# Performance work log

Hardware: AMD Instinct MI355X
Metric: run time of the kernel (lower is better)

Reference implementation:

```python
import jax, jax.numpy as jnp
import numpy as np

COORD_W, EDGE_W, COUNT_W, REG_W, CONTRA_W = 1.0, 2.0, 0.1, 0.001, 0.1
MARGIN = 1.0


def setup_inputs() -> dict:
    key = jax.random.key(0)
    ks = jax.random.split(key, 6)
    B, N, D, C = 16, 1024, 128, 2
    return {
        "predicted_coords": jax.random.normal(ks[0], (B, N, C), jnp.float32),
        "points": jax.random.normal(ks[1], (B, N, C), jnp.float32),
        "adjacency_logits": jax.random.normal(ks[2], (B, N, N), jnp.float32),
        "adjacency": jax.random.bernoulli(ks[3], 0.1, (B, N, N)).astype(jnp.float32),
        "node_masks": jnp.ones((B, N), jnp.float32),  # all nodes valid -> n_actual = N
        "predicted_count": jax.random.normal(ks[4], (B, 1), jnp.float32),
        "node_features": jax.random.normal(ks[5], (B, N, D), jnp.float32),
    }


def _bce_with_logits(logits, targets):
    # mean-reduced, numerically stable (matches F.binary_cross_entropy_with_logits)
    return jnp.mean(jnp.maximum(logits, 0.0) - logits * targets
                    + jnp.log1p(jnp.exp(-jnp.abs(logits))))


def _smooth_l1(pred, target):
    d = jnp.abs(pred - target)
    return jnp.mean(jnp.where(d < 1.0, 0.5 * d * d, d - 0.5))


def _contrastive_sample(features, adj):
    # features: [N, D], adj: [N, N]. torch.cdist pairwise euclidean via gram trick.
    nrm = jnp.sum(features * features, axis=-1)              # [N]
    sq = jnp.maximum(nrm[:, None] + nrm[None, :]
                     - 2.0 * (features @ features.T), 0.0)   # [N, N] squared dists
    n = features.shape[0]
    eye = jnp.eye(n, dtype=bool)
    pos_mask = adj > 0.5
    neg_mask = (adj <= 0.5) & (~eye)
    # positive term: mean of distances**2 over positive pairs == mean squared dist
    pos = jnp.sum(jnp.where(pos_mask, sq, 0.0)) / jnp.maximum(jnp.sum(pos_mask), 1)
    dist = jnp.sqrt(jnp.maximum(sq, 1e-12))
    hinge = jnp.square(jax.nn.relu(MARGIN - dist))
    neg = jnp.sum(jnp.where(neg_mask, hinge, 0.0)) / jnp.maximum(jnp.sum(neg_mask), 1)
    return pos + neg


def reference(predicted_coords, points, adjacency_logits, adjacency,
              node_masks, predicted_count, node_features):
    # node_masks are all ones, so the per-sample [:n_actual] slicing is the
    # full tensor; per-sample MSE/BCE means averaged over batch equal global means.
    coord_loss = jnp.mean(jnp.square(predicted_coords - points))
    edge_loss = _bce_with_logits(adjacency_logits, adjacency)
    actual_counts = jnp.sum(node_masks, axis=1)              # [B]
    count_loss = _smooth_l1(predicted_count[:, 0], actual_counts)
    reg_loss = jnp.mean(jnp.square(node_features))
    # contrastive path uses targets['adjacency'] (no predicted_adjacency key)
    contra_loss = jnp.mean(jax.vmap(_contrastive_sample)(node_features, adjacency))
    total = (COORD_W * coord_loss + EDGE_W * edge_loss + COUNT_W * count_loss
             + REG_W * reg_loss + CONTRA_W * contra_loss)
    return total, coord_loss, edge_loss, count_loss, reg_loss, contra_loss
```

## Files before the change

### kernel.cpp

```cpp
#include <hip/hip_runtime.h>
#include <hip/hip_bf16.h>

#define NN 1024
#define DD 128
#define TS 64
#define PITCH 136

#define WS_COORD 0
#define WS_REG   1
#define WS_BCE   2
#define WS_POSN  3
#define WS_POSC  19
#define WS_NEGS  35
#define WS_PDIAG 51
#define WS_CROSS 67
#define WS_CNT   83
#define WS_NORM  112

typedef __bf16 bf16_t;
typedef bf16_t bf16x8 __attribute__((ext_vector_type(8)));
typedef float  f32x4  __attribute__((ext_vector_type(4)));

__global__ __launch_bounds__(256) void prep(
    const float* __restrict__ feat, const float* __restrict__ pcoord,
    const float* __restrict__ pts,  const float* __restrict__ masks,
    float* __restrict__ ws) {
  __shared__ float red[4][3];
  const int bx = blockIdx.x;
  const int b = bx >> 3, slab = bx & 7;
  const int t = threadIdx.x, lane = t & 63, w = t >> 6;
  const int sub = lane >> 4, lq = lane & 15;
  const float* fb = feat + (size_t)b * NN * DD;

  float reg = 0.f;
  #pragma unroll
  for (int it = 0; it < 8; ++it) {
    const int node = slab * 128 + it * 16 + w * 4 + sub;
    const float4* src = (const float4*)(fb + (size_t)node * DD) + lq * 2;
    float4 u = src[0], v = src[1];
    float s = u.x*u.x + u.y*u.y + u.z*u.z + u.w*u.w
            + v.x*v.x + v.y*v.y + v.z*v.z + v.w*v.w;
    s += __shfl_xor(s, 1); s += __shfl_xor(s, 2);
    s += __shfl_xor(s, 4); s += __shfl_xor(s, 8);
    if (lq == 0) { ws[WS_NORM + b * NN + node] = s; reg += s; }
  }
  const int ci = bx * 256 + t;
  const float d = pcoord[ci] - pts[ci];
  float coord = d * d;
  float cnt = (t < 128) ? masks[b * NN + slab * 128 + t] : 0.f;

  #pragma unroll
  for (int o = 32; o; o >>= 1) {
    coord += __shfl_xor(coord, o);
    reg   += __shfl_xor(reg, o);
    cnt   += __shfl_xor(cnt, o);
  }
  if (lane == 0) { red[w][0] = coord; red[w][1] = reg; red[w][2] = cnt; }
  __syncthreads();
  if (t == 0) {
    float c = 0.f, r = 0.f, n = 0.f;
    for (int i = 0; i < 4; ++i) { c += red[i][0]; r += red[i][1]; n += red[i][2]; }
    atomicAdd(&ws[WS_COORD], c);
    atomicAdd(&ws[WS_REG], r);
    atomicAdd(&ws[WS_CNT + b], n);
  }
}

__global__ __launch_bounds__(256, 4) void mega(
    const float* __restrict__ logits, const float* __restrict__ adj,
    const float* __restrict__ feat, float* __restrict__ ws) {
  __shared__ __align__(16) char smem[2 * TS * PITCH * sizeof(bf16_t)];
  __shared__ float red[4][6];
  bf16_t* lsA = (bf16_t*)smem;
  bf16_t* lsB = (bf16_t*)(smem + TS * PITCH * sizeof(bf16_t));

  const int bx = blockIdx.x;
  const int sel = bx % 3;
  const int t = threadIdx.x, lane = t & 63, wave = t >> 6;

  if (sel == 0) {
    const int sid = bx / 3;
    const int b = sid >> 7, rblk = sid & 127;
    const size_t base = ((size_t)b * NN + (size_t)rblk * 8) * NN;
    const float4* Lr = (const float4*)(logits + base);
    const float4* Ar = (const float4*)(adj + base);
    const float* nrm = ws + WS_NORM + b * NN;

    float4 Lb[8], Ab[8];
    #pragma unroll
    for (int r = 0; r < 8; ++r) Lb[r] = Lr[r * 256 + t];
    #pragma unroll
    for (int r = 0; r < 8; ++r) Ab[r] = Ar[r * 256 + t];
    const float4 nj = *(const float4*)(nrm + t * 4);
    float ni[8];
    #pragma unroll
    for (int r = 0; r < 8; ++r) ni[r] = nrm[rblk * 8 + r];
    __builtin_amdgcn_sched_barrier(0);

    float bce = 0.f, posc = 0.f, posn = 0.f, pdiag = 0.f;
    #pragma unroll
    for (int r = 0; r < 8; ++r) {
      const float4 L = Lb[r], A = Ab[r];
      bce += fmaxf(L.x, 0.f) - L.x * A.x + __logf(1.f + __expf(-fabsf(L.x)));
      bce += fmaxf(L.y, 0.f) - L.y * A.y + __logf(1.f + __expf(-fabsf(L.y)));
      bce += fmaxf(L.z, 0.f) - L.z * A.z + __logf(1.f + __expf(-fabsf(L.z)));
      bce += fmaxf(L.w, 0.f) - L.w * A.w + __logf(1.f + __expf(-fabsf(L.w)));
      const float px = (A.x > 0.5f) ? 1.f : 0.f;
      const float py = (A.y > 0.5f) ? 1.f : 0.f;
      const float pz = (A.z > 0.5f) ? 1.f : 0.f;
      const float pw = (A.w > 0.5f) ? 1.f : 0.f;
      posc += px + py + pz + pw;
      posn += px * (ni[r] + nj.x) + py * (ni[r] + nj.y)
            + pz * (ni[r] + nj.z) + pw * (ni[r] + nj.w);
      const int grow = rblk * 8 + r;
      const int e = grow & 3;
      const float av = (e == 0) ? A.x : (e == 1) ? A.y : (e == 2) ? A.z : A.w;
      pdiag += (((grow >> 2) == t) && (av > 0.5f)) ? 1.f : 0.f;
    }
    #pragma unroll
    for (int o = 32; o; o >>= 1) {
      bce   += __shfl_xor(bce, o);
      posc  += __shfl_xor(posc, o);
      posn  += __shfl_xor(posn, o);
      pdiag += __shfl_xor(pdiag, o);
    }
    if (lane == 0) {
      red[wave][0] = bce; red[wave][1] = posc;
      red[wave][2] = posn; red[wave][3] = pdiag;
    }
    __syncthreads();
    if (t == 0) {
      float s0 = 0.f, s1 = 0.f, s2 = 0.f, s3 = 0.f;
      for (int i = 0; i < 4; ++i) {
        s0 += red[i][0]; s1 += red[i][1]; s2 += red[i][2]; s3 += red[i][3];
      }
      atomicAdd(&ws[WS_BCE], s0);
      atomicAdd(&ws[WS_POSC + b], s1);
      atomicAdd(&ws[WS_POSN + b], s2);
      atomicAdd(&ws[WS_PDIAG + b], s3);
    }
    return;
  }

  const int gid = (bx / 3) * 2 + (sel - 1);
  const int bm = ((gid & 7) << 9) | (gid >> 3);
  const int b = bm >> 8, tid = bm & 255;
  const int ti = (tid >> 4) << 6, tj = (tid & 15) << 6;
  const int lrow = lane & 15, quad = lane >> 4;
  const float* fb = feat + (size_t)b * NN * DD;
  const float* nrm = ws + WS_NORM + b * NN;

  const int rbase = wave * 16 + quad * 4;
  const int grow0 = ti + rbase;
  const float* ap = adj + (size_t)b * NN * NN + (size_t)grow0 * NN + (tj + lrow);
  float Af[4][4];
  #pragma unroll
  for (int r = 0; r < 4; ++r)
    #pragma unroll
    for (int fc = 0; fc < 4; ++fc)
      Af[fc][r] = ap[(size_t)r * NN + fc * 16];
  const float4 niv = *(const float4*)(nrm + grow0);
  float njv[4];
  #pragma unroll
  for (int fc = 0; fc < 4; ++fc) njv[fc] = nrm[tj + fc * 16 + lrow];
  __builtin_amdgcn_sched_barrier(0);

  #pragma unroll
  for (int it = 0; it < 8; ++it) {
    const int cid = it * 256 + t;
    const int tile = cid >> 10;
    const int sub = cid & 1023;
    const int row = sub >> 4;
    const int c8 = sub & 15;
    const float* src = fb + (size_t)((tile ? tj : ti) + row) * DD + c8 * 8;
    const float4 u = *(const float4*)src;
    const float4 v = *(const float4*)(src + 4);
    bf16x8 pk;
    pk[0]=(bf16_t)u.x; pk[1]=(bf16_t)u.y; pk[2]=(bf16_t)u.z; pk[3]=(bf16_t)u.w;
    pk[4]=(bf16_t)v.x; pk[5]=(bf16_t)v.y; pk[6]=(bf16_t)v.z; pk[7]=(bf16_t)v.w;
    *(bf16x8*)((tile ? lsB : lsA) + row * PITCH + c8 * 8) = pk;
  }
  __syncthreads();

  f32x4 acc[4];
  #pragma unroll
  for (int fc = 0; fc < 4; ++fc) acc[fc] = (f32x4){0.f, 0.f, 0.f, 0.f};
  #pragma unroll
  for (int k0 = 0; k0 < DD; k0 += 32) {
    const int kc = k0 + quad * 8;
    const bf16x8 aF = *(const bf16x8*)&lsA[(wave * 16 + lrow) * PITCH + kc];
    #pragma unroll
    for (int fc = 0; fc < 4; ++fc) {
      const bf16x8 bF = *(const bf16x8*)&lsB[(fc * 16 + lrow) * PITCH + kc];
      acc[fc] = __builtin_amdgcn_mfma_f32_16x16x32_bf16(aF, bF, acc[fc], 0, 0, 0);
    }
  }

  float cross = 0.f, negs = 0.f;
  #pragma unroll
  for (int fc = 0; fc < 4; ++fc) {
    const int gcol = tj + fc * 16 + lrow;
    #pragma unroll
    for (int r = 0; r < 4; ++r) {
      const float a = Af[fc][r];
      const float g = acc[fc][r];
      if (a > 0.5f) {
        cross += g;
      } else {
        const int grow = grow0 + r;
        const float ni = (r == 0) ? niv.x : (r == 1) ? niv.y : (r == 2) ? niv.z : niv.w;
        const float sq = ni + njv[fc] - 2.f * g;
        if (sq < 1.f && grow != gcol) {
          const float dd = sqrtf(fmaxf(sq, 1e-12f));
          const float h = 1.f - dd;
          negs += h * h;
        }
      }
    }
  }
  #pragma unroll
  for (int o = 32; o; o >>= 1) {
    cross += __shfl_xor(cross, o);
    negs  += __shfl_xor(negs, o);
  }
  if (lane == 0) { red[wave][0] = cross; red[wave][1] = negs; }
  __syncthreads();
  if (t == 0) {
    float s0 = 0.f, s1 = 0.f;
    for (int i = 0; i < 4; ++i) { s0 += red[i][0]; s1 += red[i][1]; }
    atomicAdd(&ws[WS_CROSS + b], s0);
    atomicAdd(&ws[WS_NEGS + b], s1);
  }
}

__global__ void finalize(const float* __restrict__ ws, const float* __restrict__ pcount,
                         float* __restrict__ out) {
  if (threadIdx.x != 0 || blockIdx.x != 0) return;
  const float coord = ws[WS_COORD] / 32768.f;
  const float reg   = ws[WS_REG] / 2097152.f;
  const float edge  = ws[WS_BCE] / 16777216.f;
  float cntl = 0.f, contra = 0.f;
  for (int b = 0; b < 16; ++b) {
    const float d = fabsf(pcount[b] - ws[WS_CNT + b]);
    cntl += (d < 1.f) ? 0.5f * d * d : d - 0.5f;
    const float posc = ws[WS_POSC + b];
    const float pos = (ws[WS_POSN + b] - 2.f * ws[WS_CROSS + b]) / fmaxf(posc, 1.f);
    const float negc = 1024.f * 1024.f - 1024.f - (posc - ws[WS_PDIAG + b]);
    const float neg = ws[WS_NEGS + b] / fmaxf(negc, 1.f);
    contra += pos + neg;
  }
  cntl *= (1.f / 16.f);
  contra *= (1.f / 16.f);
  const float total = coord + 2.f * edge + 0.1f * cntl + 0.001f * reg + 0.1f * contra;
  out[0] = total; out[1] = coord; out[2] = edge;
  out[3] = cntl;  out[4] = reg;   out[5] = contra;
}

extern "C" void kernel_launch(void* const* d_in, const int* in_sizes, int n_in,
                              void* d_out, int out_size, void* d_ws, size_t ws_size,
                              hipStream_t stream) {
  (void)in_sizes; (void)n_in; (void)out_size; (void)ws_size;
  const float* pcoord = (const float*)d_in[0];
  const float* pts    = (const float*)d_in[1];
  const float* logits = (const float*)d_in[2];
  const float* adj    = (const float*)d_in[3];
  const float* masks  = (const float*)d_in[4];
  const float* pcount = (const float*)d_in[5];
  const float* nf     = (const float*)d_in[6];
  float* ws  = (float*)d_ws;
  float* out = (float*)d_out;

  hipMemsetAsync(ws, 0, WS_NORM * sizeof(float), stream);
  prep<<<128, 256, 0, stream>>>(nf, pcoord, pts, masks, ws);
  mega<<<6144, 256, 0, stream>>>(logits, adj, nf, ws);
  finalize<<<1, 64, 0, stream>>>(ws, pcount, out);
}
```

Baseline: 217.8 us.

## Split fused mega kernel into streaming BCE kernel and separate gram-tile kernel

Splits the interleaved mega kernel into two launches: a streaming kernel that handles BCE and positive-pair statistics, and a gram-tile kernel that computes the contrastive distance tiles. The streaming kernel now covers 16 strided rows per block using software double-buffered float4 loads, so it has more bytes in flight per thread and fewer blocks. This removes the block-type divergence and lets each kernel use its own occupancy profile. In exchange it adds an extra launch and serializes the two phases, and adjacency is read twice without overlap between them.

```diff
diff --git a/kernel.cpp b/kernel.cpp
--- a/kernel.cpp
+++ b/kernel.cpp
@@ -66,86 +66,103 @@
   }
 }
 
-__global__ __launch_bounds__(256, 4) void mega(
+__global__ __launch_bounds__(256, 4) void stream_pipe(
     const float* __restrict__ logits, const float* __restrict__ adj,
-    const float* __restrict__ feat, float* __restrict__ ws) {
+    float* __restrict__ ws) {
+  __shared__ float red[4][4];
+  const int bx = blockIdx.x;
+  const int b = bx & 15, bb = bx >> 4;
+  const int t = threadIdx.x, lane = t & 63, w = t >> 6;
+  const size_t base4 = (size_t)b * (NN * NN / 4);
+  const float4* Lp = (const float4*)logits + base4;
+  const float4* Ap = (const float4*)adj + base4;
+  const float* nrm = ws + WS_NORM + b * NN;
+  const int tb = bb * 256 + t;
+
+  const float4 nj = ((const float4*)nrm)[t];
+  float ni[16];
+  #pragma unroll
+  for (int k = 0; k < 16; ++k) ni[k] = nrm[bb + k * 64];
+
+  float bce = 0.f, posc = 0.f, posn = 0.f, pdiag = 0.f;
+
+#define CONSUME(PL, PA, KB) do {                                              \
+    _Pragma("unroll")                                                         \
+    for (int k = 0; k < 4; ++k) {                                             \
+      const float4 L = PL[k], A = PA[k];                                      \
+      const int row = bb + ((KB) + k) * 64;                                   \
+      const float nv = ni[(KB) + k];                                          \
+      bce += fmaxf(L.x, 0.f) - L.x * A.x + __logf(1.f + __expf(-fabsf(L.x))); \
+      bce += fmaxf(L.y, 0.f) - L.y * A.y + __logf(1.f + __expf(-fabsf(L.y))); \
+      bce += fmaxf(L.z, 0.f) - L.z * A.z + __logf(1.f + __expf(-fabsf(L.z))); \
+      bce += fmaxf(L.w, 0.f) - L.w * A.w + __logf(1.f + __expf(-fabsf(L.w))); \
+      const float px = (A.x > 0.5f) ? 1.f : 0.f;                              \
+      const float py = (A.y > 0.5f) ? 1.f : 0.f;                              \
+      const float pz = (A.z > 0.5f) ? 1.f : 0.f;                              \
+      const float pw = (A.w > 0.5f) ? 1.f : 0.f;                              \
+      posc += px + py + pz + pw;                                              \
+      posn += px * (nv + nj.x) + py * (nv + nj.y)                             \
+            + pz * (nv + nj.z) + pw * (nv + nj.w);                            \
+      const int e = row & 3;                                                  \
+      const float av = (e == 0) ? A.x : (e == 1) ? A.y : (e == 2) ? A.z : A.w;\
+      pdiag += (((row >> 2) == t) && (av > 0.5f)) ? 1.f : 0.f;                \
+    } } while (0)
+
+  float4 PL0[4], PA0[4], PL1[4], PA1[4];
+  #pragma unroll
+  for (int k = 0; k < 4; ++k) { PL0[k] = Lp[tb + k * 16384]; PA0[k] = Ap[tb + k * 16384]; }
+  __builtin_amdgcn_sched_barrier(0);
+  #pragma unroll
+  for (int k = 0; k < 4; ++k) { PL1[k] = Lp[tb + (k + 4) * 16384]; PA1[k] = Ap[tb + (k + 4) * 16384]; }
+  __builtin_amdgcn_sched_barrier(0);
+  CONSUME(PL0, PA0, 0);
+  #pragma unroll
+  for (int k = 0; k < 4; ++k) { PL0[k] = Lp[tb + (k + 8) * 16384]; PA0[k] = Ap[tb + (k + 8) * 16384]; }
+  __builtin_amdgcn_sched_barrier(0);
+  CONSUME(PL1, PA1, 4);
+  #pragma unroll
+  for (int k = 0; k < 4; ++k) { PL1[k] = Lp[tb + (k + 12) * 16384]; PA1[k] = Ap[tb + (k + 12) * 16384]; }
+  __builtin_amdgcn_sched_barrier(0);
+  CONSUME(PL0, PA0, 8);
+  CONSUME(PL1, PA1, 12);
+#undef CONSUME
+
+  #pragma unroll
+  for (int o = 32; o; o >>= 1) {
+    bce   += __shfl_xor(bce, o);
+    posc  += __shfl_xor(posc, o);
+    posn  += __shfl_xor(posn, o);
+    pdiag += __shfl_xor(pdiag, o);
+  }
+  if (lane == 0) {
+    red[w][0] = bce; red[w][1] = posc; red[w][2] = posn; red[w][3] = pdiag;
+  }
+  __syncthreads();
+  if (t == 0) {
+    float s0 = 0.f, s1 = 0.f, s2 = 0.f, s3 = 0.f;
+    for (int i = 0; i < 4; ++i) {
+      s0 += red[i][0]; s1 += red[i][1]; s2 += red[i][2]; s3 += red[i][3];
+    }
+    atomicAdd(&ws[WS_BCE], s0);
+    atomicAdd(&ws[WS_POSC + b], s1);
+    atomicAdd(&ws[WS_POSN + b], s2);
+    atomicAdd(&ws[WS_PDIAG + b], s3);
+  }
+}
+
+__global__ __launch_bounds__(256, 4) void gram_tiles(
+    const float* __restrict__ adj, const float* __restrict__ feat,
+    float* __restrict__ ws) {
   __shared__ __align__(16) char smem[2 * TS * PITCH * sizeof(bf16_t)];
-  __shared__ float red[4][6];
+  __shared__ float red[4][2];
   bf16_t* lsA = (bf16_t*)smem;
   bf16_t* lsB = (bf16_t*)(smem + TS * PITCH * sizeof(bf16_t));
 
-  const int bx = blockIdx.x;
-  const int sel = bx % 3;
-  const int t = threadIdx.x, lane = t & 63, wave = t >> 6;
-
-  if (sel == 0) {
-    const int sid = bx / 3;
-    const int b = sid >> 7, rblk = sid & 127;
-    const size_t base = ((size_t)b * NN + (size_t)rblk * 8) * NN;
-    const float4* Lr = (const float4*)(logits + base);
-    const float4* Ar = (const float4*)(adj + base);
-    const float* nrm = ws + WS_NORM + b * NN;
-
-    float4 Lb[8], Ab[8];
-    #pragma unroll
-    for (int r = 0; r < 8; ++r) Lb[r] = Lr[r * 256 + t];
-    #pragma unroll
-    for (int r = 0; r < 8; ++r) Ab[r] = Ar[r * 256 + t];
-    const float4 nj = *(const float4*)(nrm + t * 4);
-    float ni[8];
-    #pragma unroll
-    for (int r = 0; r < 8; ++r) ni[r] = nrm[rblk * 8 + r];
-    __builtin_amdgcn_sched_barrier(0);
-
-    float bce = 0.f, posc = 0.f, posn = 0.f, pdiag = 0.f;
-    #pragma unroll
-    for (int r = 0; r < 8; ++r) {
-      const float4 L = Lb[r], A = Ab[r];
-      bce += fmaxf(L.x, 0.f) - L.x * A.x + __logf(1.f + __expf(-fabsf(L.x)));
-      bce += fmaxf(L.y, 0.f) - L.y * A.y + __logf(1.f + __expf(-fabsf(L.y)));
-      bce += fmaxf(L.z, 0.f) - L.z * A.z + __logf(1.f + __expf(-fabsf(L.z)));
-      bce += fmaxf(L.w, 0.f) - L.w * A.w + __logf(1.f + __expf(-fabsf(L.w)));
-      const float px = (A.x > 0.5f) ? 1.f : 0.f;
-      const float py = (A.y > 0.5f) ? 1.f : 0.f;
-      const float pz = (A.z > 0.5f) ? 1.f : 0.f;
-      const float pw = (A.w > 0.5f) ? 1.f : 0.f;
-      posc += px + py + pz + pw;
-      posn += px * (ni[r] + nj.x) + py * (ni[r] + nj.y)
-            + pz * (ni[r] + nj.z) + pw * (ni[r] + nj.w);
-      const int grow = rblk * 8 + r;
-      const int e = grow & 3;
-      const float av = (e == 0) ? A.x : (e == 1) ? A.y : (e == 2) ? A.z : A.w;
-      pdiag += (((grow >> 2) == t) && (av > 0.5f)) ? 1.f : 0.f;
-    }
-    #pragma unroll
-    for (int o = 32; o; o >>= 1) {
-      bce   += __shfl_xor(bce, o);
-      posc  += __shfl_xor(posc, o);
-      posn  += __shfl_xor(posn, o);
-      pdiag += __shfl_xor(pdiag, o);
-    }
-    if (lane == 0) {
-      red[wave][0] = bce; red[wave][1] = posc;
-      red[wave][2] = posn; red[wave][3] = pdiag;
-    }
-    __syncthreads();
-    if (t == 0) {
-      float s0 = 0.f, s1 = 0.f, s2 = 0.f, s3 = 0.f;
-      for (int i = 0; i < 4; ++i) {
-        s0 += red[i][0]; s1 += red[i][1]; s2 += red[i][2]; s3 += red[i][3];
-      }
-      atomicAdd(&ws[WS_BCE], s0);
-      atomicAdd(&ws[WS_POSC + b], s1);
-      atomicAdd(&ws[WS_POSN + b], s2);
-      atomicAdd(&ws[WS_PDIAG + b], s3);
-    }
-    return;
-  }
-
-  const int gid = (bx / 3) * 2 + (sel - 1);
+  const int gid = blockIdx.x;
   const int bm = ((gid & 7) << 9) | (gid >> 3);
   const int b = bm >> 8, tid = bm & 255;
   const int ti = (tid >> 4) << 6, tj = (tid & 15) << 6;
+  const int t = threadIdx.x, lane = t & 63, wave = t >> 6;
   const int lrow = lane & 15, quad = lane >> 4;
   const float* fb = feat + (size_t)b * NN * DD;
   const float* nrm = ws + WS_NORM + b * NN;
@@ -272,6 +289,7 @@
 
   hipMemsetAsync(ws, 0, WS_NORM * sizeof(float), stream);
   prep<<<128, 256, 0, stream>>>(nf, pcoord, pts, masks, ws);
-  mega<<<6144, 256, 0, stream>>>(logits, adj, nf, ws);
+  stream_pipe<<<1024, 256, 0, stream>>>(logits, adj, ws);
+  gram_tiles<<<4096, 256, 0, stream>>>(adj, nf, ws);
   finalize<<<1, 64, 0, stream>>>(ws, pcount, out);
 }
```

After: 257.7 us. +18.3%, slower.
